# Optimization experiments

Hardware: AMD Instinct MI355X
Metric: run time of the kernel (lower is better)

## Reference

```python
import jax, jax.numpy as jnp
import numpy as np


def setup_inputs() -> dict:
    key = jax.random.key(0)
    ks = jax.random.split(key, 10)
    B, N, F, H = 4, 512, 64, 4
    x = jax.random.normal(ks[0], (B, N, F), dtype=jnp.float32)
    adj = jax.random.uniform(ks[1], (N, N), dtype=jnp.float32)
    s = 1.0 / np.sqrt(F)
    Wq = jax.random.normal(ks[2], (F, F * H), dtype=jnp.float32) * s
    bq = jnp.zeros((F * H,), dtype=jnp.float32)
    Wk = jax.random.normal(ks[3], (F, F * H), dtype=jnp.float32) * s
    bk = jnp.zeros((F * H,), dtype=jnp.float32)
    Wlin = jax.random.normal(ks[4], (H, F), dtype=jnp.float32) * (1.0 / np.sqrt(H))
    blin = jnp.zeros((F,), dtype=jnp.float32)
    Wfc = jax.random.normal(ks[5], (F, F), dtype=jnp.float32) * s
    bfc = jnp.zeros((F,), dtype=jnp.float32)
    return {"x": x, "adj": adj, "Wq": Wq, "bq": bq, "Wk": Wk, "bk": bk,
            "Wlin": Wlin, "blin": blin, "Wfc": Wfc, "bfc": bfc}


def reference(x, adj, Wq, bq, Wk, bk, Wlin, blin, Wfc, bfc):
    B, N, F = x.shape
    H = Wlin.shape[0]
    # multi-head attention matrix (value projection is computed but unused in the original)
    q = (x @ Wq + bq).reshape(B, N, H, F)  # [B,N,H,F]
    k = (x @ Wk + bk).reshape(B, N, H, F)
    scores = jnp.einsum('bihf,bjhf->bhij', q, k) / jnp.sqrt(jnp.float32(F))
    attn = jax.nn.softmax(scores, axis=-1)  # [B,H,N,N]
    # linear over heads: [B,N,N,H] @ [H,F] -> [B,N,N,F]
    SV2 = jnp.einsum('bhij,hf->bijf', attn, Wlin) + blin
    # symmetric normalization of (adj + I)
    A = adj + jnp.eye(N, dtype=adj.dtype)
    d = jnp.sum(A, axis=1) ** -0.5
    noradj = d[:, None] * A * d[None, :]  # [N,N]
    # sum over dim 1 (source index i) of noradj[i,j]*SV2[b,i,j,f]*x[b,j,f]
    S = jnp.einsum('ij,bijf->bjf', noradj, SV2)
    sx = x * S  # [B,N,F]
    out = jnp.einsum('ij,bjf->bif', noradj, sx)
    out = out @ Wfc + bfc
    return jax.nn.relu(out)
```

## Files before the change

kernel.cpp:

```cpp
#include <hip/hip_runtime.h>
#include <math.h>

#define NN 512
#define FF 64
#define HH 4


__global__ __launch_bounds__(256) void k_s1(const float* __restrict__ x,
                                            const float* __restrict__ Wq,
                                            const float* __restrict__ bq,
                                            const float* __restrict__ Wk,
                                            const float* __restrict__ bk,
                                            const float* __restrict__ adj,
                                            float* __restrict__ q_t,
                                            float* __restrict__ k_t,
                                            float* __restrict__ dinv,
                                            float* __restrict__ T,
                                            float* __restrict__ cvec) {
    __shared__ float x_lds[4][64];
    int blk = blockIdx.x, tid = threadIdx.x;
    int wave = tid >> 6, lane = tid & 63;

    if (blk < 512 && wave == 0) {
        float acc = 0.f;
#pragma unroll
        for (int k = 0; k < 8; ++k) acc += adj[(long)blk * NN + k * 64 + lane];
        for (int o = 32; o > 0; o >>= 1) acc += __shfl_xor(acc, o);
        if (lane == 0) dinv[blk] = 1.0f / sqrtf(acc + 1.0f);
    }
    if (blk < 128 && wave == 1) T[blk * 64 + lane] = 0.f;
    if (blk < 8 && wave == 2) cvec[blk * 64 + lane] = 0.f;

    int b = blk >> 8, rest = blk & 255, isK = rest >> 7, itile = rest & 127;
    int i0 = itile * 4;
    x_lds[tid >> 6][tid & 63] = x[((long)b * NN + i0 + (tid >> 6)) * FF + (tid & 63)];
    __syncthreads();
    const float* W = isK ? Wk : Wq;
    float bv = (isK ? bk : bq)[tid];
    float a0 = bv, a1 = bv, a2 = bv, a3 = bv;
    for (int cc = 0; cc < 64; ++cc) {
        float w = W[cc * 256 + tid];
        a0 = fmaf(x_lds[0][cc], w, a0);
        a1 = fmaf(x_lds[1][cc], w, a1);
        a2 = fmaf(x_lds[2][cc], w, a2);
        a3 = fmaf(x_lds[3][cc], w, a3);
    }
    int h = tid >> 6, f = tid & 63;
    float* dst = (isK ? k_t : q_t) + ((long)(b * HH + h) * NN + i0) * FF + f;
    dst[0] = a0; dst[FF] = a1; dst[2 * FF] = a2; dst[3 * FF] = a3;
}

__global__ __launch_bounds__(512) void k_s2(const float* __restrict__ q_t,
                                            const float* __restrict__ k_t,
                                            const float* __restrict__ adj,
                                            const float* __restrict__ dinv,
                                            float* __restrict__ T,
                                            float* __restrict__ cvec) {
    __shared__ float ql[16 * 68];
    __shared__ float kl[512 * 16];
    __shared__ float redm[8][16];
    __shared__ float redz[8][16];
    int blk = blockIdx.x, tid = threadIdx.x;
    int bh = blk >> 5, itile = blk & 31;
    int i0 = itile * 16;
    int wv = tid >> 6;
    int ig = tid & 7, jg = tid >> 3;

    if (tid < 256) {
        int r = tid >> 4, c4 = tid & 15;
        *(float4*)&ql[r * 68 + c4 * 4] =
            *(const float4*)(q_t + ((long)bh * NN + i0 + r) * FF + c4 * 4);
    }

    float acc[2][8];
#pragma unroll
    for (int ii = 0; ii < 2; ++ii)
#pragma unroll
        for (int jj = 0; jj < 8; ++jj) acc[ii][jj] = 0.f;

    const float* kb = k_t + (long)bh * NN * FF;
#pragma unroll
    for (int cc = 0; cc < 4; ++cc) {
#pragma unroll
        for (int w = 0; w < 4; ++w) {
            int v = w * 512 + tid;
            int row = v >> 2, c4 = v & 3;
            int slot = c4 ^ ((row >> 3) & 3);
            *(float4*)&kl[row * 16 + slot * 4] =
                *(const float4*)(kb + (long)row * FF + cc * 16 + c4 * 4);
        }
        __syncthreads();
#pragma unroll
        for (int k4 = 0; k4 < 4; ++k4) {
            float4 qf[2], kf[8];
#pragma unroll
            for (int ii = 0; ii < 2; ++ii)
                qf[ii] = *(const float4*)&ql[(ig * 2 + ii) * 68 + cc * 16 + k4 * 4];
#pragma unroll
            for (int jj = 0; jj < 8; ++jj) {
                int j = jg * 8 + jj;
                int slot = k4 ^ ((j >> 3) & 3);
                kf[jj] = *(const float4*)&kl[j * 16 + slot * 4];
            }
#pragma unroll
            for (int ii = 0; ii < 2; ++ii)
#pragma unroll
                for (int jj = 0; jj < 8; ++jj) {
                    acc[ii][jj] = fmaf(qf[ii].x, kf[jj].x, acc[ii][jj]);
                    acc[ii][jj] = fmaf(qf[ii].y, kf[jj].y, acc[ii][jj]);
                    acc[ii][jj] = fmaf(qf[ii].z, kf[jj].z, acc[ii][jj]);
                    acc[ii][jj] = fmaf(qf[ii].w, kf[jj].w, acc[ii][jj]);
                }
        }
        __syncthreads();
    }

#pragma unroll
    for (int w = 0; w < 4; ++w) {
        int v = w * 512 + tid;
        int r = v >> 7, c4 = v & 127;
        *(float4*)&kl[r * 512 + c4 * 4] =
            *(const float4*)(adj + (long)(i0 + r) * NN + c4 * 4);
    }

    const float scale = 0.125f;
    float m[2], Zi[2];
#pragma unroll
    for (int ii = 0; ii < 2; ++ii) {
        float v = acc[ii][0];
#pragma unroll
        for (int jj = 1; jj < 8; ++jj) v = fmaxf(v, acc[ii][jj]);
        v = fmaxf(v, __shfl_xor(v, 8));
        v = fmaxf(v, __shfl_xor(v, 16));
        v = fmaxf(v, __shfl_xor(v, 32));
        if ((tid & 63) < 8) redm[wv][ig * 2 + ii] = v;
    }
    __syncthreads();
#pragma unroll
    for (int ii = 0; ii < 2; ++ii) {
        int row = ig * 2 + ii;
        float v = redm[0][row];
#pragma unroll
        for (int w = 1; w < 8; ++w) v = fmaxf(v, redm[w][row]);
        m[ii] = v;
    }
#pragma unroll
    for (int ii = 0; ii < 2; ++ii) {
        float z = 0.f;
#pragma unroll
        for (int jj = 0; jj < 8; ++jj) {
            float p = expf((acc[ii][jj] - m[ii]) * scale);
            acc[ii][jj] = p;
            z += p;
        }
        z += __shfl_xor(z, 8);
        z += __shfl_xor(z, 16);
        z += __shfl_xor(z, 32);
        if ((tid & 63) < 8) redz[wv][ig * 2 + ii] = z;
    }
    __syncthreads();
#pragma unroll
    for (int ii = 0; ii < 2; ++ii) {
        int row = ig * 2 + ii;
        float z = redz[0][row];
#pragma unroll
        for (int w = 1; w < 8; ++w) z += redz[w][row];
        Zi[ii] = 1.0f / z;
    }

    float di[2];
    di[0] = dinv[i0 + ig * 2];
    di[1] = dinv[i0 + ig * 2 + 1];
    float cs[8], cw[8];
#pragma unroll
    for (int jj = 0; jj < 8; ++jj) { cs[jj] = 0.f; cw[jj] = 0.f; }
#pragma unroll
    for (int ii = 0; ii < 2; ++ii) {
        int irow = ig * 2 + ii;
        int gi = i0 + irow;
        float av[8];
        *(float4*)&av[0] = *(const float4*)&kl[irow * 512 + jg * 8];
        *(float4*)&av[4] = *(const float4*)&kl[irow * 512 + jg * 8 + 4];
        float dz = di[ii] * Zi[ii];
#pragma unroll
        for (int jj = 0; jj < 8; ++jj) {
            int j = jg * 8 + jj;
            float a = av[jj] + (gi == j ? 1.f : 0.f);
            cs[jj] = fmaf(di[ii] * a * Zi[ii], acc[ii][jj], cs[jj]);
            cw[jj] = fmaf(di[ii], a, cw[jj]);
        }
        (void)dz;
    }
#pragma unroll
    for (int jj = 0; jj < 8; ++jj) {
        float v = cs[jj];
        v += __shfl_xor(v, 1);
        v += __shfl_xor(v, 2);
        v += __shfl_xor(v, 4);
        cs[jj] = v;
    }
    if (bh == 0) {
#pragma unroll
        for (int jj = 0; jj < 8; ++jj) {
            float w = cw[jj];
            w += __shfl_xor(w, 1);
            w += __shfl_xor(w, 2);
            w += __shfl_xor(w, 4);
            cw[jj] = w;
        }
    }
    if (ig == 0) {
#pragma unroll
        for (int jj = 0; jj < 8; ++jj) {
            int j = jg * 8 + jj;
            atomicAdd(&T[bh * NN + j], cs[jj] * dinv[j]);
        }
        if (bh == 0) {
#pragma unroll
            for (int jj = 0; jj < 8; ++jj)
                atomicAdd(&cvec[jg * 8 + jj], cw[jj]);
        }
    }
}

__global__ __launch_bounds__(256) void k_s3(const float* __restrict__ x,
                                            const float* __restrict__ T,
                                            const float* __restrict__ Wlin,
                                            const float* __restrict__ blin,
                                            const float* __restrict__ cvec,
                                            const float* __restrict__ adj,
                                            const float* __restrict__ dinv,
                                            const float* __restrict__ Wfc,
                                            const float* __restrict__ bfc,
                                            float* __restrict__ out) {
    __shared__ float4 u4_l[NN];
    __shared__ float  u0_l[NN];
    __shared__ float2 ad_l[NN];
    __shared__ float part[4][2][64];
    __shared__ float m_lds[2][64];
    __shared__ float part2[4][2][64];
    int blk = blockIdx.x, tid = threadIdx.x;
    int b = blk >> 8, itile = blk & 255;
    int i0 = itile * 2;

    for (int jj = tid; jj < NN; jj += 256) {
        float dj = dinv[jj];
        u0_l[jj] = dj * dj * cvec[jj];
        u4_l[jj] = make_float4(dj * T[(b * HH + 0) * NN + jj],
                               dj * T[(b * HH + 1) * NN + jj],
                               dj * T[(b * HH + 2) * NN + jj],
                               dj * T[(b * HH + 3) * NN + jj]);
        ad_l[jj] = make_float2(adj[(long)i0 * NN + jj] + (i0 == jj ? 1.f : 0.f),
                               adj[(long)(i0 + 1) * NN + jj] + (i0 + 1 == jj ? 1.f : 0.f));
    }
    __syncthreads();

    int f = tid & 63, jc = tid >> 6;
    int jb = jc * 128;
    float blf = blin[f];
    float4 wl = make_float4(Wlin[f], Wlin[64 + f], Wlin[128 + f], Wlin[192 + f]);
    const float* xb = x + (long)b * NN * FF + f;
    float a0 = 0.f, a1 = 0.f;
#pragma unroll 4
    for (int j = jb; j < jb + 128; ++j) {
        float xv = xb[(long)j * FF];
        float4 u = u4_l[j];
        float2 ad = ad_l[j];
        float S = blf * u0_l[j];
        S = fmaf(wl.x, u.x, S);
        S = fmaf(wl.y, u.y, S);
        S = fmaf(wl.z, u.z, S);
        S = fmaf(wl.w, u.w, S);
        float sx = xv * S;
        a0 = fmaf(ad.x, sx, a0);
        a1 = fmaf(ad.y, sx, a1);
    }
    part[jc][0][f] = a0;
    part[jc][1][f] = a1;
    __syncthreads();
    if (jc == 0) {
        m_lds[0][f] = (part[0][0][f] + part[1][0][f] + part[2][0][f] + part[3][0][f]) * dinv[i0];
        m_lds[1][f] = (part[0][1][f] + part[1][1][f] + part[2][1][f] + part[3][1][f]) * dinv[i0 + 1];
    }
    __syncthreads();
    float o0 = 0.f, o1 = 0.f;
    int c0 = jc * 16;
#pragma unroll
    for (int cc = 0; cc < 16; ++cc) {
        float w = Wfc[(c0 + cc) * FF + f];
        o0 = fmaf(m_lds[0][c0 + cc], w, o0);
        o1 = fmaf(m_lds[1][c0 + cc], w, o1);
    }
    part2[jc][0][f] = o0;
    part2[jc][1][f] = o1;
    __syncthreads();
    if (jc == 0) {
        float bb = bfc[f];
        float r0 = part2[0][0][f] + part2[1][0][f] + part2[2][0][f] + part2[3][0][f] + bb;
        float r1 = part2[0][1][f] + part2[1][1][f] + part2[2][1][f] + part2[3][1][f] + bb;
        out[((long)b * NN + i0) * FF + f]     = fmaxf(r0, 0.f);
        out[((long)b * NN + i0 + 1) * FF + f] = fmaxf(r1, 0.f);
    }
}

extern "C" void kernel_launch(void* const* d_in, const int* in_sizes, int n_in,
                              void* d_out, int out_size, void* d_ws, size_t ws_size,
                              hipStream_t stream) {
    const float* x    = (const float*)d_in[0];
    const float* adj  = (const float*)d_in[1];
    const float* Wq   = (const float*)d_in[2];
    const float* bq   = (const float*)d_in[3];
    const float* Wk   = (const float*)d_in[4];
    const float* bk   = (const float*)d_in[5];
    const float* Wlin = (const float*)d_in[6];
    const float* blin = (const float*)d_in[7];
    const float* Wfc  = (const float*)d_in[8];
    const float* bfc  = (const float*)d_in[9];
    float* out = (float*)d_out;

    float* ws   = (float*)d_ws;
    float* dinv = ws;
    float* cvec = ws + 512;
    float* T    = ws + 1024;
    float* q_t  = ws + 9216;
    float* k_t  = ws + 2106368;

    k_s1<<<dim3(1024), dim3(256), 0, stream>>>(x, Wq, bq, Wk, bk, adj, q_t, k_t, dinv, T, cvec);
    k_s2<<<dim3(512), dim3(512), 0, stream>>>(q_t, k_t, adj, dinv, T, cvec);
    k_s3<<<dim3(1024), dim3(256), 0, stream>>>(x, T, Wlin, blin, cvec, adj, dinv, Wfc, bfc, out);
}
```

Before: 120.9 us.

## Retile all three stages for more rows per block and vectorized weights

The projection kernel now handles 8 rows per block with float4 weight loads and two rows per thread, folding the degree and zeroing work into the batch-0 blocks. The attention kernel doubles its query tile to 32 rows and reads adj straight from global memory instead of staging it in LDS. The output kernel handles 4 rows per block, computes S on the fly from global memory with no LDS staging, adds the diagonal term separately, and computes a full 64-wide Wfc dot per thread. The aim is to amortise loads and launch overhead over more rows, at the cost of fewer blocks and more registers per thread.

New measurement: 126.2 us. 4.4% more time.

```diff
diff --git a/kernel.cpp b/kernel.cpp
--- a/kernel.cpp
+++ b/kernel.cpp
@@ -6,7 +6,7 @@
 #define HH 4
 
 
-__global__ __launch_bounds__(256) void k_s1(const float* __restrict__ x,
+__global__ __launch_bounds__(512) void k_s1(const float* __restrict__ x,
                                             const float* __restrict__ Wq,
                                             const float* __restrict__ bq,
                                             const float* __restrict__ Wk,
@@ -17,37 +17,50 @@
                                             float* __restrict__ dinv,
                                             float* __restrict__ T,
                                             float* __restrict__ cvec) {
-    __shared__ float x_lds[4][64];
+    __shared__ float xl[8][64];
     int blk = blockIdx.x, tid = threadIdx.x;
     int wave = tid >> 6, lane = tid & 63;
-
-    if (blk < 512 && wave == 0) {
+    int b = blk >> 6, itile = blk & 63;
+    int i0 = itile * 8;
+
+    xl[tid >> 6][tid & 63] = x[((long)b * NN + i0 + (tid >> 6)) * FF + (tid & 63)];
+
+    if (b == 0) {
+        int gi = i0 + wave;
         float acc = 0.f;
 #pragma unroll
-        for (int k = 0; k < 8; ++k) acc += adj[(long)blk * NN + k * 64 + lane];
+        for (int k = 0; k < 8; ++k) acc += adj[(long)gi * NN + k * 64 + lane];
         for (int o = 32; o > 0; o >>= 1) acc += __shfl_xor(acc, o);
-        if (lane == 0) dinv[blk] = 1.0f / sqrtf(acc + 1.0f);
-    }
-    if (blk < 128 && wave == 1) T[blk * 64 + lane] = 0.f;
-    if (blk < 8 && wave == 2) cvec[blk * 64 + lane] = 0.f;
-
-    int b = blk >> 8, rest = blk & 255, isK = rest >> 7, itile = rest & 127;
-    int i0 = itile * 4;
-    x_lds[tid >> 6][tid & 63] = x[((long)b * NN + i0 + (tid >> 6)) * FF + (tid & 63)];
-    __syncthreads();
+        if (lane == 0) dinv[gi] = 1.0f / sqrtf(acc + 1.0f);
+    }
+    if (blk < 16) T[blk * 512 + tid] = 0.f;
+    if (blk == 0) cvec[tid] = 0.f;
+    __syncthreads();
+
+    int rg = tid >> 7;
+    int cg = tid & 127;
+    int col4 = cg * 4;
+    int isK = col4 >> 8;
+    int colq = col4 & 255;
     const float* W = isK ? Wk : Wq;
-    float bv = (isK ? bk : bq)[tid];
-    float a0 = bv, a1 = bv, a2 = bv, a3 = bv;
+    const float* bias = isK ? bk : bq;
+    float4 bv = *(const float4*)(bias + colq);
+    float4 a0 = bv, a1 = bv;
+    const float* xr0 = &xl[rg * 2][0];
+    const float* xr1 = &xl[rg * 2 + 1][0];
+#pragma unroll 8
     for (int cc = 0; cc < 64; ++cc) {
-        float w = W[cc * 256 + tid];
-        a0 = fmaf(x_lds[0][cc], w, a0);
-        a1 = fmaf(x_lds[1][cc], w, a1);
-        a2 = fmaf(x_lds[2][cc], w, a2);
-        a3 = fmaf(x_lds[3][cc], w, a3);
-    }
-    int h = tid >> 6, f = tid & 63;
-    float* dst = (isK ? k_t : q_t) + ((long)(b * HH + h) * NN + i0) * FF + f;
-    dst[0] = a0; dst[FF] = a1; dst[2 * FF] = a2; dst[3 * FF] = a3;
+        float4 w = *(const float4*)(W + cc * 256 + colq);
+        float x0 = xr0[cc], x1 = xr1[cc];
+        a0.x = fmaf(x0, w.x, a0.x); a0.y = fmaf(x0, w.y, a0.y);
+        a0.z = fmaf(x0, w.z, a0.z); a0.w = fmaf(x0, w.w, a0.w);
+        a1.x = fmaf(x1, w.x, a1.x); a1.y = fmaf(x1, w.y, a1.y);
+        a1.z = fmaf(x1, w.z, a1.z); a1.w = fmaf(x1, w.w, a1.w);
+    }
+    int h = colq >> 6, f = colq & 63;
+    float* dst = (isK ? k_t : q_t) + ((long)(b * HH + h) * NN + (i0 + rg * 2)) * FF + f;
+    *(float4*)dst = a0;
+    *(float4*)(dst + FF) = a1;
 }
 
 __global__ __launch_bounds__(512) void k_s2(const float* __restrict__ q_t,
@@ -56,25 +69,25 @@
                                             const float* __restrict__ dinv,
                                             float* __restrict__ T,
                                             float* __restrict__ cvec) {
-    __shared__ float ql[16 * 68];
+    __shared__ float ql[32 * 68];
     __shared__ float kl[512 * 16];
-    __shared__ float redm[8][16];
-    __shared__ float redz[8][16];
+    __shared__ float redm[8][32];
+    __shared__ float redz[8][32];
     int blk = blockIdx.x, tid = threadIdx.x;
-    int bh = blk >> 5, itile = blk & 31;
-    int i0 = itile * 16;
-    int wv = tid >> 6;
+    int bh = blk >> 4, itile = blk & 15;
+    int i0 = itile * 32;
+    int wv = tid >> 6, lane = tid & 63;
     int ig = tid & 7, jg = tid >> 3;
 
-    if (tid < 256) {
+    {
         int r = tid >> 4, c4 = tid & 15;
         *(float4*)&ql[r * 68 + c4 * 4] =
             *(const float4*)(q_t + ((long)bh * NN + i0 + r) * FF + c4 * 4);
     }
 
-    float acc[2][8];
-#pragma unroll
-    for (int ii = 0; ii < 2; ++ii)
+    float acc[4][8];
+#pragma unroll
+    for (int ii = 0; ii < 4; ++ii)
 #pragma unroll
         for (int jj = 0; jj < 8; ++jj) acc[ii][jj] = 0.f;
 
@@ -92,10 +105,10 @@
         __syncthreads();
 #pragma unroll
         for (int k4 = 0; k4 < 4; ++k4) {
-            float4 qf[2], kf[8];
-#pragma unroll
-            for (int ii = 0; ii < 2; ++ii)
-                qf[ii] = *(const float4*)&ql[(ig * 2 + ii) * 68 + cc * 16 + k4 * 4];
+            float4 qf[4], kf[8];
+#pragma unroll
+            for (int ii = 0; ii < 4; ++ii)
+                qf[ii] = *(const float4*)&ql[(ig * 4 + ii) * 68 + cc * 16 + k4 * 4];
 #pragma unroll
             for (int jj = 0; jj < 8; ++jj) {
                 int j = jg * 8 + jj;
@@ -103,7 +116,7 @@
                 kf[jj] = *(const float4*)&kl[j * 16 + slot * 4];
             }
 #pragma unroll
-            for (int ii = 0; ii < 2; ++ii)
+            for (int ii = 0; ii < 4; ++ii)
 #pragma unroll
                 for (int jj = 0; jj < 8; ++jj) {
                     acc[ii][jj] = fmaf(qf[ii].x, kf[jj].x, acc[ii][jj]);
@@ -115,37 +128,29 @@
         __syncthreads();
     }
 
-#pragma unroll
-    for (int w = 0; w < 4; ++w) {
-        int v = w * 512 + tid;
-        int r = v >> 7, c4 = v & 127;
-        *(float4*)&kl[r * 512 + c4 * 4] =
-            *(const float4*)(adj + (long)(i0 + r) * NN + c4 * 4);
-    }
-
     const float scale = 0.125f;
-    float m[2], Zi[2];
-#pragma unroll
-    for (int ii = 0; ii < 2; ++ii) {
+    float m[4], Zi[4];
+#pragma unroll
+    for (int ii = 0; ii < 4; ++ii) {
         float v = acc[ii][0];
 #pragma unroll
         for (int jj = 1; jj < 8; ++jj) v = fmaxf(v, acc[ii][jj]);
         v = fmaxf(v, __shfl_xor(v, 8));
         v = fmaxf(v, __shfl_xor(v, 16));
         v = fmaxf(v, __shfl_xor(v, 32));
-        if ((tid & 63) < 8) redm[wv][ig * 2 + ii] = v;
-    }
-    __syncthreads();
-#pragma unroll
-    for (int ii = 0; ii < 2; ++ii) {
-        int row = ig * 2 + ii;
+        if (lane < 8) redm[wv][ig * 4 + ii] = v;
+    }
+    __syncthreads();
+#pragma unroll
+    for (int ii = 0; ii < 4; ++ii) {
+        int row = ig * 4 + ii;
         float v = redm[0][row];
 #pragma unroll
         for (int w = 1; w < 8; ++w) v = fmaxf(v, redm[w][row]);
         m[ii] = v;
     }
 #pragma unroll
-    for (int ii = 0; ii < 2; ++ii) {
+    for (int ii = 0; ii < 4; ++ii) {
         float z = 0.f;
 #pragma unroll
         for (int jj = 0; jj < 8; ++jj) {
@@ -156,40 +161,36 @@
         z += __shfl_xor(z, 8);
         z += __shfl_xor(z, 16);
         z += __shfl_xor(z, 32);
-        if ((tid & 63) < 8) redz[wv][ig * 2 + ii] = z;
-    }
-    __syncthreads();
-#pragma unroll
-    for (int ii = 0; ii < 2; ++ii) {
-        int row = ig * 2 + ii;
+        if (lane < 8) redz[wv][ig * 4 + ii] = z;
+    }
+    __syncthreads();
+#pragma unroll
+    for (int ii = 0; ii < 4; ++ii) {
+        int row = ig * 4 + ii;
         float z = redz[0][row];
 #pragma unroll
         for (int w = 1; w < 8; ++w) z += redz[w][row];
         Zi[ii] = 1.0f / z;
     }
 
-    float di[2];
-    di[0] = dinv[i0 + ig * 2];
-    di[1] = dinv[i0 + ig * 2 + 1];
     float cs[8], cw[8];
 #pragma unroll
     for (int jj = 0; jj < 8; ++jj) { cs[jj] = 0.f; cw[jj] = 0.f; }
 #pragma unroll
-    for (int ii = 0; ii < 2; ++ii) {
-        int irow = ig * 2 + ii;
-        int gi = i0 + irow;
+    for (int ii = 0; ii < 4; ++ii) {
+        int gi = i0 + ig * 4 + ii;
+        float di = dinv[gi];
         float av[8];
-        *(float4*)&av[0] = *(const float4*)&kl[irow * 512 + jg * 8];
-        *(float4*)&av[4] = *(const float4*)&kl[irow * 512 + jg * 8 + 4];
-        float dz = di[ii] * Zi[ii];
+        *(float4*)&av[0] = *(const float4*)(adj + (long)gi * NN + jg * 8);
+        *(float4*)&av[4] = *(const float4*)(adj + (long)gi * NN + jg * 8 + 4);
+        float dz = di * Zi[ii];
 #pragma unroll
         for (int jj = 0; jj < 8; ++jj) {
             int j = jg * 8 + jj;
             float a = av[jj] + (gi == j ? 1.f : 0.f);
-            cs[jj] = fmaf(di[ii] * a * Zi[ii], acc[ii][jj], cs[jj]);
-            cw[jj] = fmaf(di[ii], a, cw[jj]);
-        }
-        (void)dz;
+            cs[jj] = fmaf(dz * a, acc[ii][jj], cs[jj]);
+            cw[jj] = fmaf(di, a, cw[jj]);
+        }
     }
 #pragma unroll
     for (int jj = 0; jj < 8; ++jj) {
@@ -224,83 +225,69 @@
 }
 
 __global__ __launch_bounds__(256) void k_s3(const float* __restrict__ x,
+                                            const float* __restrict__ adj,
+                                            const float* __restrict__ dinv,
+                                            const float* __restrict__ cvec,
                                             const float* __restrict__ T,
                                             const float* __restrict__ Wlin,
                                             const float* __restrict__ blin,
-                                            const float* __restrict__ cvec,
-                                            const float* __restrict__ adj,
-                                            const float* __restrict__ dinv,
                                             const float* __restrict__ Wfc,
                                             const float* __restrict__ bfc,
                                             float* __restrict__ out) {
-    __shared__ float4 u4_l[NN];
-    __shared__ float  u0_l[NN];
-    __shared__ float2 ad_l[NN];
-    __shared__ float part[4][2][64];
-    __shared__ float m_lds[2][64];
-    __shared__ float part2[4][2][64];
+    __shared__ float part[4][4][64];
+    __shared__ float m_lds[4][64];
     int blk = blockIdx.x, tid = threadIdx.x;
-    int b = blk >> 8, itile = blk & 255;
-    int i0 = itile * 2;
-
-    for (int jj = tid; jj < NN; jj += 256) {
-        float dj = dinv[jj];
-        u0_l[jj] = dj * dj * cvec[jj];
-        u4_l[jj] = make_float4(dj * T[(b * HH + 0) * NN + jj],
-                               dj * T[(b * HH + 1) * NN + jj],
-                               dj * T[(b * HH + 2) * NN + jj],
-                               dj * T[(b * HH + 3) * NN + jj]);
-        ad_l[jj] = make_float2(adj[(long)i0 * NN + jj] + (i0 == jj ? 1.f : 0.f),
-                               adj[(long)(i0 + 1) * NN + jj] + (i0 + 1 == jj ? 1.f : 0.f));
-    }
-    __syncthreads();
-
+    int b = blk >> 7, itile = blk & 127;
+    int i0 = itile * 4;
     int f = tid & 63, jc = tid >> 6;
-    int jb = jc * 128;
+
     float blf = blin[f];
     float4 wl = make_float4(Wlin[f], Wlin[64 + f], Wlin[128 + f], Wlin[192 + f]);
     const float* xb = x + (long)b * NN * FF + f;
-    float a0 = 0.f, a1 = 0.f;
+    const float* Tb = T + (long)b * HH * NN;
+    const float* ar0 = adj + (long)(i0 + 0) * NN;
+    const float* ar1 = adj + (long)(i0 + 1) * NN;
+    const float* ar2 = adj + (long)(i0 + 2) * NN;
+    const float* ar3 = adj + (long)(i0 + 3) * NN;
+
+    float a0 = 0.f, a1 = 0.f, a2 = 0.f, a3 = 0.f;
+    int jb = jc * 128;
 #pragma unroll 4
     for (int j = jb; j < jb + 128; ++j) {
-        float xv = xb[(long)j * FF];
-        float4 u = u4_l[j];
-        float2 ad = ad_l[j];
-        float S = blf * u0_l[j];
-        S = fmaf(wl.x, u.x, S);
-        S = fmaf(wl.y, u.y, S);
-        S = fmaf(wl.z, u.z, S);
-        S = fmaf(wl.w, u.w, S);
-        float sx = xv * S;
-        a0 = fmaf(ad.x, sx, a0);
-        a1 = fmaf(ad.y, sx, a1);
-    }
-    part[jc][0][f] = a0;
-    part[jc][1][f] = a1;
-    __syncthreads();
-    if (jc == 0) {
-        m_lds[0][f] = (part[0][0][f] + part[1][0][f] + part[2][0][f] + part[3][0][f]) * dinv[i0];
-        m_lds[1][f] = (part[0][1][f] + part[1][1][f] + part[2][1][f] + part[3][1][f]) * dinv[i0 + 1];
-    }
-    __syncthreads();
-    float o0 = 0.f, o1 = 0.f;
-    int c0 = jc * 16;
-#pragma unroll
-    for (int cc = 0; cc < 16; ++cc) {
-        float w = Wfc[(c0 + cc) * FF + f];
-        o0 = fmaf(m_lds[0][c0 + cc], w, o0);
-        o1 = fmaf(m_lds[1][c0 + cc], w, o1);
-    }
-    part2[jc][0][f] = o0;
-    part2[jc][1][f] = o1;
-    __syncthreads();
-    if (jc == 0) {
-        float bb = bfc[f];
-        float r0 = part2[0][0][f] + part2[1][0][f] + part2[2][0][f] + part2[3][0][f] + bb;
-        float r1 = part2[0][1][f] + part2[1][1][f] + part2[2][1][f] + part2[3][1][f] + bb;
-        out[((long)b * NN + i0) * FF + f]     = fmaxf(r0, 0.f);
-        out[((long)b * NN + i0 + 1) * FF + f] = fmaxf(r1, 0.f);
-    }
+        float dj = dinv[j];
+        float S = blf * (dj * dj * cvec[j]);
+        S = fmaf(wl.x, dj * Tb[j], S);
+        S = fmaf(wl.y, dj * Tb[NN + j], S);
+        S = fmaf(wl.z, dj * Tb[2 * NN + j], S);
+        S = fmaf(wl.w, dj * Tb[3 * NN + j], S);
+        float sx = xb[(long)j * FF] * S;
+        a0 = fmaf(ar0[j], sx, a0);
+        a1 = fmaf(ar1[j], sx, a1);
+        a2 = fmaf(ar2[j], sx, a2);
+        a3 = fmaf(ar3[j], sx, a3);
+    }
+    part[jc][0][f] = a0; part[jc][1][f] = a1;
+    part[jc][2][f] = a2; part[jc][3][f] = a3;
+    __syncthreads();
+
+    int r = jc;
+    int gi = i0 + r;
+    float djq = dinv[gi];
+    float Sq = blf * (djq * djq * cvec[gi]);
+    Sq = fmaf(wl.x, djq * Tb[gi], Sq);
+    Sq = fmaf(wl.y, djq * Tb[NN + gi], Sq);
+    Sq = fmaf(wl.z, djq * Tb[2 * NN + gi], Sq);
+    Sq = fmaf(wl.w, djq * Tb[3 * NN + gi], Sq);
+    float sx_id = xb[(long)gi * FF] * Sq;
+    m_lds[r][f] = (part[0][r][f] + part[1][r][f] + part[2][r][f] + part[3][r][f]
+                   + sx_id) * djq;
+    __syncthreads();
+
+    float o = bfc[f];
+#pragma unroll
+    for (int cc = 0; cc < 64; ++cc)
+        o = fmaf(m_lds[r][cc], Wfc[cc * FF + f], o);
+    out[((long)b * NN + gi) * FF + f] = fmaxf(o, 0.f);
 }
 
 extern "C" void kernel_launch(void* const* d_in, const int* in_sizes, int n_in,
@@ -325,7 +312,7 @@
     float* q_t  = ws + 9216;
     float* k_t  = ws + 2106368;
 
-    k_s1<<<dim3(1024), dim3(256), 0, stream>>>(x, Wq, bq, Wk, bk, adj, q_t, k_t, dinv, T, cvec);
-    k_s2<<<dim3(512), dim3(512), 0, stream>>>(q_t, k_t, adj, dinv, T, cvec);
-    k_s3<<<dim3(1024), dim3(256), 0, stream>>>(x, T, Wlin, blin, cvec, adj, dinv, Wfc, bfc, out);
+    k_s1<<<dim3(256), dim3(512), 0, stream>>>(x, Wq, bq, Wk, bk, adj, q_t, k_t, dinv, T, cvec);
+    k_s2<<<dim3(256), dim3(512), 0, stream>>>(q_t, k_t, adj, dinv, T, cvec);
+    k_s3<<<dim3(512), dim3(256), 0, stream>>>(x, adj, dinv, cvec, T, Wlin, blin, Wfc, bfc, out);
 }
```
